# Performance work log

Hardware: AMD Instinct MI355X
Metric: run time of the kernel (lower is better)

Reference implementation:

```python
import jax, jax.numpy as jnp
import numpy as np

N = 20000      # nodes
E = 320000     # edges
S = 256        # scalar (0e) channels of irreps_feature
F = 960        # full irreps_feature dim (256x0e+128x1e+64x2e)
NB = 32        # number_of_basis
CUT = 5.0      # max_radius


def setup_inputs() -> dict:
    key = jax.random.key(0)
    ks = jax.random.split(key, 24)
    def w(k, shape):
        return jax.random.normal(k, shape, jnp.float32) / np.sqrt(shape[0])
    return {
        "node_feature": jax.random.normal(ks[0], (N, F), jnp.float32),
        "pos": jax.random.normal(ks[1], (N, 3), jnp.float32),
        "edge_index": jax.random.randint(ks[2], (2, E), 0, N),
        "W_ai1": w(ks[3], (S, S)), "b_ai1": jnp.zeros((S,), jnp.float32),
        "W_ai2": w(ks[4], (S, 1)), "b_ai2": jnp.zeros((1,), jnp.float32),
        "W_ci1": w(ks[5], (S, S)), "b_ci1": jnp.zeros((S,), jnp.float32),
        "W_ci2": w(ks[6], (S, 1)), "b_ci2": jnp.zeros((1,), jnp.float32),
        "W_sc": w(ks[7], (S, S)), "b_sc": jnp.zeros((S,), jnp.float32),
        "W_ed": w(ks[8], (NB, S)), "b_ed": jnp.zeros((S,), jnp.float32),
        "W_b1": w(ks[9], (3 * S, S)), "b_b1": jnp.zeros((S,), jnp.float32),
        "W_b2": w(ks[10], (S, 1)), "b_b2": jnp.zeros((1,), jnp.float32),
    }


def _rbf(d):
    # ExpNormalSmearing (torchmd-net), cutoff_lower=0, cutoff_upper=CUT, non-trainable
    start = np.exp(-CUT)
    means = jnp.linspace(start, 1.0, NB, dtype=jnp.float32)
    beta = jnp.float32(((2.0 / NB) * (1.0 - start)) ** -2)
    cosine_cut = 0.5 * (jnp.cos(np.pi * d / CUT) + 1.0) * (d < CUT)
    return cosine_cut[:, None] * jnp.exp(-beta * (jnp.exp(-d)[:, None] - means) ** 2)


def reference(node_feature, pos, edge_index,
              W_ai1, b_ai1, W_ai2, b_ai2,
              W_ci1, b_ci1, W_ci2, b_ci2,
              W_sc, b_sc, W_ed, b_ed,
              W_b1, b_b1, W_b2, b_b2):
    # LinearRS(irreps_feature -> 0e) only touches the 0e block (first S channels)
    scal = node_feature[:, :S]
    silu = jax.nn.silu

    log_ai = silu(scal @ W_ai1 + b_ai1) @ W_ai2 + b_ai2          # [N,1]
    ai = jnp.exp(log_ai)
    log_ci = silu(scal @ W_ci1 + b_ci1) @ W_ci2 + b_ci2          # [N,1]
    ci = jnp.exp(log_ci)

    src, dst = edge_index[0], edge_index[1]
    rel = pos[dst] - pos[src]                                     # [E,3]
    norm = jnp.linalg.norm(rel, axis=1, keepdims=True)            # [E,1]
    rhat = rel / (norm + 1e-8)
    emb = _rbf(norm[:, 0])                                        # [E,NB]

    node_sc = scal @ W_sc + b_sc                                  # project once, gather [N,S]
    src_f = node_sc[src]
    dst_f = node_sc[dst]
    edge_f = emb @ W_ed + b_ed
    edge_feature = jnp.concatenate([src_f, dst_f, edge_f], axis=-1)  # [E,3S]
    bij = silu(edge_feature @ W_b1 + b_b1) @ W_b2 + b_b2          # [E,1]

    # edge softmax over incoming edges of dst, with extra ci mass
    bmax = jax.ops.segment_max(bij, dst, num_segments=N)
    bmax = jnp.where(jnp.isneginf(bmax), 0.0, bmax)
    bij_exp = jnp.exp(bij - bmax[dst])
    bsum = jax.ops.segment_sum(bij_exp, dst, num_segments=N) + ci  # [N,1]
    gamma = bij_exp / (bsum[dst] + 1e-7)                           # [E,1]

    bij_prime = gamma * ai[dst]                                    # [E,1]
    outer = rhat[:, :, None] * rhat[:, None, :]                    # [E,3,3]
    contrib = jax.ops.segment_sum(bij_prime[:, :, None] * outer, dst, num_segments=N)  # [N,3,3]

    eye3 = jnp.eye(3, dtype=pos.dtype)
    sigma = ai[:, :, None] * eye3 - contrib + 1e-6 * eye3          # [N,3,3]
    sum_gamma = jax.ops.segment_sum(gamma, dst, num_segments=N)    # [N,1]
    return sigma, ai, sum_gamma
```

## Files before the change

kernel.cpp:

```cpp
#include <hip/hip_runtime.h>
#include <math.h>

#define N_NODES 20000
#define E_EDGES 320000
#define F_DIM   960
#define S_DIM   256
#define QTAB    2048
#define ASTRIDE 264
#define CAP     64
#define CPAD    66

typedef __attribute__((ext_vector_type(8))) short short8;
typedef __attribute__((ext_vector_type(4))) float f32x4;

__device__ __forceinline__ float siluf(float x) {
    return x / (1.0f + __expf(-x));
}

__device__ __forceinline__ unsigned short bf16rn(float x) {
    unsigned u = __float_as_uint(x);
    return (unsigned short)((u + 0x7FFFu + ((u >> 16) & 1u)) >> 16);
}

__device__ __forceinline__ void bf16x8_to_f32(short8 v8, float* o) {
    union { short8 s; uint4 u; } cv; cv.s = v8;
    o[0] = __uint_as_float(cv.u.x << 16);
    o[1] = __uint_as_float(cv.u.x & 0xffff0000u);
    o[2] = __uint_as_float(cv.u.y << 16);
    o[3] = __uint_as_float(cv.u.y & 0xffff0000u);
    o[4] = __uint_as_float(cv.u.z << 16);
    o[5] = __uint_as_float(cv.u.z & 0xffff0000u);
    o[6] = __uint_as_float(cv.u.w << 16);
    o[7] = __uint_as_float(cv.u.w & 0xffff0000u);
}

__global__ void prep_kernel(const float* __restrict__ W_sc, const float* __restrict__ W_ed,
                            const float* __restrict__ W_b1, const float* __restrict__ b_sc,
                            const float* __restrict__ b_ed, const float* __restrict__ b_b1,
                            const float* __restrict__ W_ai1, const float* __restrict__ W_ci1,
                            float* __restrict__ Bcat, float* __restrict__ We, float* __restrict__ c0,
                            int* __restrict__ cnt)
{
    int idx = blockIdx.x * 256 + threadIdx.x;
    if (idx < N_NODES) cnt[idx] = 0;
    if (idx < 256 * 1024) {
        int k = idx >> 10, j = idx & 1023;
        float s = 0.0f;
        if (j < 256) {
            for (int m = 0; m < 256; ++m) s += W_sc[k * 256 + m] * W_b1[m * 256 + j];
        } else if (j < 512) {
            int jj = j - 256;
            for (int m = 0; m < 256; ++m) s += W_sc[k * 256 + m] * W_b1[(256 + m) * 256 + jj];
        } else if (j < 768) {
            s = W_ai1[k * 256 + (j - 512)];
        } else {
            s = W_ci1[k * 256 + (j - 768)];
        }
        Bcat[idx] = s;
    } else if (idx < 256 * 1024 + 32 * 256) {
        int t = idx - 256 * 1024;
        int p = t >> 8, j = t & 255;
        float s = 0.0f;
        for (int m = 0; m < 256; ++m) s += W_ed[p * 256 + m] * W_b1[(512 + m) * 256 + j];
        We[t] = s;
    } else if (idx < 256 * 1024 + 32 * 256 + 256) {
        int j = idx - 256 * 1024 - 32 * 256;
        float s = b_b1[j];
        for (int m = 0; m < 256; ++m) {
            s += b_sc[m] * (W_b1[m * 256 + j] + W_b1[(256 + m) * 256 + j]);
            s += b_ed[m] * W_b1[(512 + m) * 256 + j];
        }
        c0[j] = s;
    }
}

__global__ void aux_kernel(const int* __restrict__ ei, int* __restrict__ cnt, int* __restrict__ rank,
                           const float* __restrict__ Bcat, unsigned short* __restrict__ Bpack,
                           const float* __restrict__ We, unsigned short* __restrict__ Tab,
                           const float* __restrict__ nf, unsigned short* __restrict__ scalp)
{
    int b = blockIdx.x;
    if (b < 1250) {
        int i = b * 256 + threadIdx.x;
        rank[i] = atomicAdd(&cnt[ei[E_EDGES + i]], 1);
    } else if (b < 1378) {
        int idx = (b - 1250) * 256 + threadIdx.x;
        int kq = idx & 3, j = (idx >> 2) & 1023, t = idx >> 12;
        #pragma unroll
        for (int jj = 0; jj < 8; ++jj)
            Bpack[idx * 8 + jj] = bf16rn(Bcat[(t * 32 + kq * 8 + jj) * 1024 + j]);
    } else if (b < 3426) {
        int idx = (b - 1378) * 256 + threadIdx.x;
        int q = idx >> 8, j = idx & 255;
        float nrm = 5.0f * (float)q / (float)(QTAB - 1);
        const float start = 0.006737946999085467f;
        const float mustep = (1.0f - start) / 31.0f;
        const float bx = (2.0f / 32.0f) * (1.0f - start);
        const float beta = 1.0f / (bx * bx);
        const float PI_F = 3.14159265358979323846f;
        float cc = (nrm < 5.0f) ? 0.5f * (cosf(PI_F * nrm * 0.2f) + 1.0f) : 0.0f;
        float t = expf(-nrm);
        float s = 0.0f;
        for (int k = 0; k < 32; ++k) {
            float dm = t - (start + (float)k * mustep);
            s += expf(-beta * dm * dm) * We[k * 256 + j];
        }
        Tab[idx] = bf16rn(cc * s);
    } else {
        int idx = (b - 3426) * 256 + threadIdx.x;
        int base = idx * 4;
        int n = base >> 8, k = base & 255;
        float4 a4 = *(const float4*)&nf[(size_t)n * F_DIM + k];
        ushort4 b4;
        b4.x = bf16rn(a4.x); b4.y = bf16rn(a4.y);
        b4.z = bf16rn(a4.z); b4.w = bf16rn(a4.w);
        *(ushort4*)&scalp[n * 256 + k] = b4;
    }
}

__global__ __launch_bounds__(1024) void scan_kernel(const int* __restrict__ cnt,
                                                    int* __restrict__ start)
{
    __shared__ int ps[1024];
    const int t = threadIdx.x;
    const int base = t * 20;
    int loc[20];
    int s = 0;
    #pragma unroll
    for (int i = 0; i < 20; ++i) {
        int n = (base + i < N_NODES) ? cnt[base + i] : 0;
        loc[i] = s; s += n;
    }
    ps[t] = s;
    __syncthreads();
    for (int off = 1; off < 1024; off <<= 1) {
        int v = (t >= off) ? ps[t - off] : 0;
        __syncthreads();
        ps[t] += v;
        __syncthreads();
    }
    int offset = ps[t] - s;
    #pragma unroll
    for (int i = 0; i < 20; ++i)
        if (base + i < N_NODES) start[base + i] = offset + loc[i];
}

__global__ void scatter_kernel(const int* __restrict__ ei, const int* __restrict__ start,
                               const int* __restrict__ rank, int* __restrict__ srcS)
{
    int i = blockIdx.x * 256 + threadIdx.x;
    if (i < E_EDGES) srcS[start[ei[E_EDGES + i]] + rank[i]] = ei[i];
}

__global__ __launch_bounds__(256) void node_mfma_kernel(
    const unsigned short* __restrict__ scalp, const unsigned short* __restrict__ Bpack,
    const float* __restrict__ c0,
    const float* __restrict__ b_ai1, const float* __restrict__ W_ai2, const float* __restrict__ b_ai2,
    const float* __restrict__ b_ci1, const float* __restrict__ W_ci2, const float* __restrict__ b_ci2,
    unsigned short* __restrict__ u, unsigned short* __restrict__ v,
    float* __restrict__ bsumseed, float* __restrict__ out_ai)
{
    __shared__ unsigned short A[32 * ASTRIDE];
    __shared__ float red[32 * 4];

    const int tid = threadIdx.x;
    const int w = tid >> 6, lane = tid & 63;
    const int bg = blockIdx.x & 3;
    const int m0 = (blockIdx.x >> 2) * 32;
    const int col16 = lane & 15, quad = lane >> 4;

    #pragma unroll
    for (int it = 0; it < 4; ++it) {
        int idx = (it * 256 + tid) * 8;
        int r = idx >> 8, c = idx & 255;
        *(uint4*)&A[r * ASTRIDE + c] = *(const uint4*)&scalp[(m0 + r) * 256 + c];
    }
    __syncthreads();

    f32x4 acc[2][4];
    #pragma unroll
    for (int mt = 0; mt < 2; ++mt)
        #pragma unroll
        for (int nt = 0; nt < 4; ++nt)
            acc[mt][nt] = (f32x4){0.0f, 0.0f, 0.0f, 0.0f};

    const int colbase = bg * 256 + w * 64;

    for (int t = 0; t < 8; ++t) {
        short8 af[2];
        #pragma unroll
        for (int mt = 0; mt < 2; ++mt)
            af[mt] = *(const short8*)&A[(mt * 16 + col16) * ASTRIDE + t * 32 + quad * 8];
        short8 bf[4];
        #pragma unroll
        for (int nt = 0; nt < 4; ++nt)
            bf[nt] = *(const short8*)&Bpack[(((t * 1024 + colbase + nt * 16 + col16) * 4) + quad) * 8];
        #pragma unroll
        for (int mt = 0; mt < 2; ++mt)
            #pragma unroll
            for (int nt = 0; nt < 4; ++nt)
                acc[mt][nt] = __builtin_amdgcn_mfma_f32_16x16x32_bf16(af[mt], bf[nt], acc[mt][nt], 0, 0, 0);
    }

    if (bg == 0) {
        #pragma unroll
        for (int nt = 0; nt < 4; ++nt) {
            int jl = w * 64 + nt * 16 + col16;
            float c0v = c0[jl];
            #pragma unroll
            for (int mt = 0; mt < 2; ++mt)
                #pragma unroll
                for (int reg = 0; reg < 4; ++reg)
                    u[(m0 + mt * 16 + quad * 4 + reg) * 256 + jl] = bf16rn(acc[mt][nt][reg] + c0v);
        }
    } else if (bg == 1) {
        #pragma unroll
        for (int nt = 0; nt < 4; ++nt) {
            int jl = w * 64 + nt * 16 + col16;
            #pragma unroll
            for (int mt = 0; mt < 2; ++mt)
                #pragma unroll
                for (int reg = 0; reg < 4; ++reg)
                    v[(m0 + mt * 16 + quad * 4 + reg) * 256 + jl] = bf16rn(acc[mt][nt][reg]);
        }
    } else {
        const float* b1 = (bg == 2) ? b_ai1 : b_ci1;
        const float* w2 = (bg == 2) ? W_ai2 : W_ci2;
        float s[2][4] = {{0, 0, 0, 0}, {0, 0, 0, 0}};
        #pragma unroll
        for (int nt = 0; nt < 4; ++nt) {
            int jl = w * 64 + nt * 16 + col16;
            float bb = b1[jl], ww = w2[jl];
            #pragma unroll
            for (int mt = 0; mt < 2; ++mt)
                #pragma unroll
                for (int reg = 0; reg < 4; ++reg)
                    s[mt][reg] += siluf(acc[mt][nt][reg] + bb) * ww;
        }
        #pragma unroll
        for (int off = 1; off < 16; off <<= 1) {
            #pragma unroll
            for (int mt = 0; mt < 2; ++mt)
                #pragma unroll
                for (int reg = 0; reg < 4; ++reg)
                    s[mt][reg] += __shfl_xor(s[mt][reg], off);
        }
        if (col16 == 0) {
            #pragma unroll
            for (int mt = 0; mt < 2; ++mt)
                #pragma unroll
                for (int reg = 0; reg < 4; ++reg)
                    red[(mt * 16 + quad * 4 + reg) * 4 + w] = s[mt][reg];
        }
        __syncthreads();
        if (tid < 32) {
            float sum = red[tid * 4] + red[tid * 4 + 1] + red[tid * 4 + 2] + red[tid * 4 + 3];
            if (bg == 2) out_ai[m0 + tid] = expf(sum + b_ai2[0]);
            else         bsumseed[m0 + tid] = expf(sum + b_ci2[0]) + 1e-7f;
        }
    }
}

__global__ __launch_bounds__(256) void edge_node_kernel(
    const int* __restrict__ start, const int* __restrict__ cnt, const int* __restrict__ srcS,
    const float* __restrict__ pos,
    const unsigned short* __restrict__ u, const unsigned short* __restrict__ v,
    const unsigned short* __restrict__ Tab, const float* __restrict__ W_b2, const float* __restrict__ b_b2,
    const float* __restrict__ bsumseed, const float* __restrict__ out_ai,
    float* __restrict__ out_sigma, float* __restrict__ out_sg)
{
    __shared__ float sb[16][CPAD];
    __shared__ float srx[16][CPAD];
    __shared__ float sry[16][CPAD];
    __shared__ float srz[16][CPAD];

    const int grp = threadIdx.x >> 4;
    const int l   = threadIdx.x & 15;
    const int g   = blockIdx.x * 16 + grp;
    const int st  = start[g];
    const int deg = min(cnt[g], CAP);

    float vch[16];
    bf16x8_to_f32(*(const short8*)&v[(size_t)g * 256 + l * 16], vch);
    bf16x8_to_f32(*(const short8*)&v[(size_t)g * 256 + l * 16 + 8], vch + 8);
    float w2c[16];
    #pragma unroll
    for (int c = 0; c < 16; c += 4)
        *(float4*)&w2c[c] = *(const float4*)&W_b2[l * 16 + c];
    const float bb2 = b_b2[0];
    const float gx = pos[3 * g + 0], gy = pos[3 * g + 1], gz = pos[3 * g + 2];
    const float xscale = (float)(QTAB - 1) * 0.2f;

    int s_cur = (deg > 0) ? srcS[st] : 0;
    float pxc = pos[3 * s_cur + 0], pyc = pos[3 * s_cur + 1], pzc = pos[3 * s_cur + 2];
    short8 u0c = *(const short8*)&u[(size_t)s_cur * 256 + l * 16];
    short8 u1c = *(const short8*)&u[(size_t)s_cur * 256 + l * 16 + 8];

    for (int i = 0; i < deg; ++i) {
        int s_nxt = (i + 1 < deg) ? srcS[st + i + 1] : s_cur;
        float pxn = pos[3 * s_nxt + 0], pyn = pos[3 * s_nxt + 1], pzn = pos[3 * s_nxt + 2];
        short8 u0n = *(const short8*)&u[(size_t)s_nxt * 256 + l * 16];
        short8 u1n = *(const short8*)&u[(size_t)s_nxt * 256 + l * 16 + 8];

        float px = gx - pxc, py = gy - pyc, pz = gz - pzc;
        float nrm = sqrtf(px * px + py * py + pz * pz);
        float inv = 1.0f / (nrm + 1e-8f);
        float rx = px * inv, ry = py * inv, rz = pz * inv;

        float x = nrm * xscale;
        int qi = (int)x;
        float f = x - (float)qi;
        if (qi >= QTAB - 1) { qi = QTAB - 2; f = 1.0f; }

        float acc = 0.0f;
        #pragma unroll
        for (int half = 0; half < 2; ++half) {
            float uf[8], t0f[8], t1f[8];
            bf16x8_to_f32(half ? u1c : u0c, uf);
            bf16x8_to_f32(*(const short8*)&Tab[(size_t)qi * 256 + l * 16 + half * 8], t0f);
            bf16x8_to_f32(*(const short8*)&Tab[(size_t)(qi + 1) * 256 + l * 16 + half * 8], t1f);
            #pragma unroll
            for (int c = 0; c < 8; ++c) {
                float h = uf[c] + vch[half * 8 + c] + t0f[c] + f * (t1f[c] - t0f[c]);
                float sig = __builtin_amdgcn_rcpf(1.0f + __expf(-h));
                acc += w2c[half * 8 + c] * h * sig;
            }
        }
        #pragma unroll
        for (int off = 1; off < 16; off <<= 1) acc += __shfl_xor(acc, off);

        if (l == 0) {
            sb[grp][i] = acc + bb2;
            srx[grp][i] = rx; sry[grp][i] = ry; srz[grp][i] = rz;
        }
        s_cur = s_nxt; pxc = pxn; pyc = pyn; pzc = pzn; u0c = u0n; u1c = u1n;
    }

    float m = -1e30f;
    for (int i = l; i < deg; i += 16) m = fmaxf(m, sb[grp][i]);
    #pragma unroll
    for (int off = 1; off < 16; off <<= 1) m = fmaxf(m, __shfl_xor(m, off));

    float ssum = 0.0f;
    for (int i = l; i < deg; i += 16) ssum += __expf(sb[grp][i] - m);
    #pragma unroll
    for (int off = 1; off < 16; off <<= 1) ssum += __shfl_xor(ssum, off);

    float invt = 1.0f / (ssum + bsumseed[g]);

    float a0 = 0, a1 = 0, a2 = 0, a3 = 0, a4 = 0, a5 = 0, a6 = 0;
    for (int i = l; i < deg; i += 16) {
        float gm = __expf(sb[grp][i] - m) * invt;
        float rx = srx[grp][i], ry = sry[grp][i], rz = srz[grp][i];
        a0 += gm * rx * rx; a1 += gm * ry * ry; a2 += gm * rz * rz;
        a3 += gm * rx * ry; a4 += gm * rx * rz; a5 += gm * ry * rz;
        a6 += gm;
    }
    #pragma unroll
    for (int off = 1; off < 16; off <<= 1) {
        a0 += __shfl_xor(a0, off); a1 += __shfl_xor(a1, off);
        a2 += __shfl_xor(a2, off); a3 += __shfl_xor(a3, off);
        a4 += __shfl_xor(a4, off); a5 += __shfl_xor(a5, off);
        a6 += __shfl_xor(a6, off);
    }

    if (l == 0) {
        float ai = out_ai[g];
        float* sg = &out_sigma[g * 9];
        float d0 = ai + 1e-6f;
        sg[0] = d0 - ai * a0;
        sg[1] = -ai * a3;
        sg[2] = -ai * a4;
        sg[3] = -ai * a3;
        sg[4] = d0 - ai * a1;
        sg[5] = -ai * a5;
        sg[6] = -ai * a4;
        sg[7] = -ai * a5;
        sg[8] = d0 - ai * a2;
        out_sg[g] = a6;
    }
}

extern "C" void kernel_launch(void* const* d_in, const int* in_sizes, int n_in,
                              void* d_out, int out_size, void* d_ws, size_t ws_size,
                              hipStream_t stream)
{
    const float* nf    = (const float*)d_in[0];
    const float* pos   = (const float*)d_in[1];
    const int*   ei    = (const int*)  d_in[2];
    const float* W_ai1 = (const float*)d_in[3];
    const float* b_ai1 = (const float*)d_in[4];
    const float* W_ai2 = (const float*)d_in[5];
    const float* b_ai2 = (const float*)d_in[6];
    const float* W_ci1 = (const float*)d_in[7];
    const float* b_ci1 = (const float*)d_in[8];
    const float* W_ci2 = (const float*)d_in[9];
    const float* b_ci2 = (const float*)d_in[10];
    const float* W_sc  = (const float*)d_in[11];
    const float* b_sc  = (const float*)d_in[12];
    const float* W_ed  = (const float*)d_in[13];
    const float* b_ed  = (const float*)d_in[14];
    const float* W_b1  = (const float*)d_in[15];
    const float* b_b1  = (const float*)d_in[16];
    const float* W_b2  = (const float*)d_in[17];
    const float* b_b2  = (const float*)d_in[18];

    char* pb = (char*)d_ws;
    auto alloc = [&](size_t bytes) -> void* {
        void* r = (void*)pb;
        pb += (bytes + 255) & ~(size_t)255;
        return r;
    };
    float*          Bcat    = (float*)         alloc(262144 * 4);
    float*          We      = (float*)         alloc(8192 * 4);
    float*          c0      = (float*)         alloc(256 * 4);
    unsigned short* Tab     = (unsigned short*)alloc((size_t)QTAB * 256 * 2);
    unsigned short* Bpack   = (unsigned short*)alloc((size_t)256 * 1024 * 2);
    unsigned short* scalp   = (unsigned short*)alloc((size_t)N_NODES * 256 * 2);
    unsigned short* u       = (unsigned short*)alloc((size_t)N_NODES * 256 * 2);
    unsigned short* v       = (unsigned short*)alloc((size_t)N_NODES * 256 * 2);
    float*          bsumseed= (float*)         alloc((size_t)N_NODES * 4);
    int*            cnt     = (int*)           alloc((size_t)N_NODES * 4);
    int*            startA  = (int*)           alloc((size_t)N_NODES * 4);
    int*            rank    = (int*)           alloc((size_t)E_EDGES * 4);
    int*            srcS    = (int*)           alloc((size_t)E_EDGES * 4);

    float* out       = (float*)d_out;
    float* out_sigma = out;
    float* out_ai    = out + N_NODES * 9;
    float* out_sg    = out + N_NODES * 10;

    prep_kernel<<<1058, 256, 0, stream>>>(W_sc, W_ed, W_b1, b_sc, b_ed, b_b1, W_ai1, W_ci1,
                                          Bcat, We, c0, cnt);
    aux_kernel<<<8426, 256, 0, stream>>>(ei, cnt, rank, Bcat, Bpack, We, Tab, nf, scalp);
    scan_kernel<<<1, 1024, 0, stream>>>(cnt, startA);
    scatter_kernel<<<1250, 256, 0, stream>>>(ei, startA, rank, srcS);
    node_mfma_kernel<<<2500, 256, 0, stream>>>(scalp, Bpack, c0, b_ai1, W_ai2, b_ai2,
                                               b_ci1, W_ci2, b_ci2, u, v, bsumseed, out_ai);
    edge_node_kernel<<<1250, 256, 0, stream>>>(startA, cnt, srcS, pos, u, v, Tab, W_b2, b_b2,
                                               bsumseed, out_ai, out_sigma, out_sg);
}
```

Measured before the change: 320.2 us.

## Split fused edge-node kernel into edge-parallel bij pass and node reduction

Replaces the per-destination sequential edge loop with an edge-parallel kernel (one 16-lane group per edge) that computes the edge logit and unit direction and scatters them into CSR order. A separate node kernel then does the softmax and outer-product reduction over the sorted float4 records. This removes the scatter kernel and the serial per-node dependency chain with its load imbalance, at the cost of an extra 5 MB write/read of intermediate edge records and reloading v per edge instead of once per node. The node kernel now handles at most 64 edges per node via 4 fixed slots, matching the existing CAP.

```diff
diff --git a/kernel.cpp b/kernel.cpp
--- a/kernel.cpp
+++ b/kernel.cpp
@@ -8,7 +8,6 @@
 #define QTAB    2048
 #define ASTRIDE 264
 #define CAP     64
-#define CPAD    66
 
 typedef __attribute__((ext_vector_type(8))) short short8;
 typedef __attribute__((ext_vector_type(4))) float f32x4;
@@ -145,13 +144,6 @@
         if (base + i < N_NODES) start[base + i] = offset + loc[i];
 }
 
-__global__ void scatter_kernel(const int* __restrict__ ei, const int* __restrict__ start,
-                               const int* __restrict__ rank, int* __restrict__ srcS)
-{
-    int i = blockIdx.x * 256 + threadIdx.x;
-    if (i < E_EDGES) srcS[start[ei[E_EDGES + i]] + rank[i]] = ei[i];
-}
-
 __global__ __launch_bounds__(256) void node_mfma_kernel(
     const unsigned short* __restrict__ scalp, const unsigned short* __restrict__ Bpack,
     const float* __restrict__ c0,
@@ -261,99 +253,114 @@
     }
 }
 
-__global__ __launch_bounds__(256) void edge_node_kernel(
-    const int* __restrict__ start, const int* __restrict__ cnt, const int* __restrict__ srcS,
+__global__ __launch_bounds__(256) void edge_bij_kernel(
+    const int* __restrict__ ei, const int* __restrict__ start, const int* __restrict__ rank,
     const float* __restrict__ pos,
     const unsigned short* __restrict__ u, const unsigned short* __restrict__ v,
-    const unsigned short* __restrict__ Tab, const float* __restrict__ W_b2, const float* __restrict__ b_b2,
+    const unsigned short* __restrict__ Tab,
+    const float* __restrict__ W_b2, const float* __restrict__ b_b2,
+    float4* __restrict__ bijS)
+{
+    const int l = threadIdx.x & 15;
+    const int e = blockIdx.x * 16 + (threadIdx.x >> 4);
+    const int src = ei[e];
+    const int dst = ei[E_EDGES + e];
+
+    float px = pos[3 * dst + 0] - pos[3 * src + 0];
+    float py = pos[3 * dst + 1] - pos[3 * src + 1];
+    float pz = pos[3 * dst + 2] - pos[3 * src + 2];
+    float nrm = sqrtf(px * px + py * py + pz * pz);
+    float inv = 1.0f / (nrm + 1e-8f);
+    float rx = px * inv, ry = py * inv, rz = pz * inv;
+
+    const float xscale = (float)(QTAB - 1) * 0.2f;
+    float x = nrm * xscale;
+    int qi = (int)x;
+    float f = x - (float)qi;
+    if (qi >= QTAB - 1) { qi = QTAB - 2; f = 1.0f; }
+
+    float w2c[16];
+    #pragma unroll
+    for (int c = 0; c < 16; c += 4)
+        *(float4*)&w2c[c] = *(const float4*)&W_b2[l * 16 + c];
+
+    short8 u0 = *(const short8*)&u[(size_t)src * 256 + l * 16];
+    short8 u1 = *(const short8*)&u[(size_t)src * 256 + l * 16 + 8];
+    short8 v0 = *(const short8*)&v[(size_t)dst * 256 + l * 16];
+    short8 v1 = *(const short8*)&v[(size_t)dst * 256 + l * 16 + 8];
+
+    float acc = 0.0f;
+    #pragma unroll
+    for (int half = 0; half < 2; ++half) {
+        float uf[8], vf[8], t0f[8], t1f[8];
+        bf16x8_to_f32(half ? u1 : u0, uf);
+        bf16x8_to_f32(half ? v1 : v0, vf);
+        bf16x8_to_f32(*(const short8*)&Tab[(size_t)qi * 256 + l * 16 + half * 8], t0f);
+        bf16x8_to_f32(*(const short8*)&Tab[(size_t)(qi + 1) * 256 + l * 16 + half * 8], t1f);
+        #pragma unroll
+        for (int c = 0; c < 8; ++c) {
+            float h = uf[c] + vf[c] + t0f[c] + f * (t1f[c] - t0f[c]);
+            float sig = __builtin_amdgcn_rcpf(1.0f + __expf(-h));
+            acc += w2c[half * 8 + c] * h * sig;
+        }
+    }
+    #pragma unroll
+    for (int off = 1; off < 16; off <<= 1) acc += __shfl_xor(acc, off);
+
+    if (l == 0) {
+        float4 o;
+        o.x = acc + b_b2[0];
+        o.y = rx; o.z = ry; o.w = rz;
+        bijS[start[dst] + rank[e]] = o;
+    }
+}
+
+__global__ __launch_bounds__(256) void node_reduce_kernel(
+    const int* __restrict__ start, const int* __restrict__ cnt,
+    const float4* __restrict__ bijS,
     const float* __restrict__ bsumseed, const float* __restrict__ out_ai,
     float* __restrict__ out_sigma, float* __restrict__ out_sg)
 {
-    __shared__ float sb[16][CPAD];
-    __shared__ float srx[16][CPAD];
-    __shared__ float sry[16][CPAD];
-    __shared__ float srz[16][CPAD];
-
     const int grp = threadIdx.x >> 4;
-    const int l   = threadIdx.x & 15;
-    const int g   = blockIdx.x * 16 + grp;
-    const int st  = start[g];
+    const int l = threadIdx.x & 15;
+    const int g = blockIdx.x * 16 + grp;
+    const int st = start[g];
     const int deg = min(cnt[g], CAP);
 
-    float vch[16];
-    bf16x8_to_f32(*(const short8*)&v[(size_t)g * 256 + l * 16], vch);
-    bf16x8_to_f32(*(const short8*)&v[(size_t)g * 256 + l * 16 + 8], vch + 8);
-    float w2c[16];
-    #pragma unroll
-    for (int c = 0; c < 16; c += 4)
-        *(float4*)&w2c[c] = *(const float4*)&W_b2[l * 16 + c];
-    const float bb2 = b_b2[0];
-    const float gx = pos[3 * g + 0], gy = pos[3 * g + 1], gz = pos[3 * g + 2];
-    const float xscale = (float)(QTAB - 1) * 0.2f;
-
-    int s_cur = (deg > 0) ? srcS[st] : 0;
-    float pxc = pos[3 * s_cur + 0], pyc = pos[3 * s_cur + 1], pzc = pos[3 * s_cur + 2];
-    short8 u0c = *(const short8*)&u[(size_t)s_cur * 256 + l * 16];
-    short8 u1c = *(const short8*)&u[(size_t)s_cur * 256 + l * 16 + 8];
-
-    for (int i = 0; i < deg; ++i) {
-        int s_nxt = (i + 1 < deg) ? srcS[st + i + 1] : s_cur;
-        float pxn = pos[3 * s_nxt + 0], pyn = pos[3 * s_nxt + 1], pzn = pos[3 * s_nxt + 2];
-        short8 u0n = *(const short8*)&u[(size_t)s_nxt * 256 + l * 16];
-        short8 u1n = *(const short8*)&u[(size_t)s_nxt * 256 + l * 16 + 8];
-
-        float px = gx - pxc, py = gy - pyc, pz = gz - pzc;
-        float nrm = sqrtf(px * px + py * py + pz * pz);
-        float inv = 1.0f / (nrm + 1e-8f);
-        float rx = px * inv, ry = py * inv, rz = pz * inv;
-
-        float x = nrm * xscale;
-        int qi = (int)x;
-        float f = x - (float)qi;
-        if (qi >= QTAB - 1) { qi = QTAB - 2; f = 1.0f; }
-
-        float acc = 0.0f;
-        #pragma unroll
-        for (int half = 0; half < 2; ++half) {
-            float uf[8], t0f[8], t1f[8];
-            bf16x8_to_f32(half ? u1c : u0c, uf);
-            bf16x8_to_f32(*(const short8*)&Tab[(size_t)qi * 256 + l * 16 + half * 8], t0f);
-            bf16x8_to_f32(*(const short8*)&Tab[(size_t)(qi + 1) * 256 + l * 16 + half * 8], t1f);
-            #pragma unroll
-            for (int c = 0; c < 8; ++c) {
-                float h = uf[c] + vch[half * 8 + c] + t0f[c] + f * (t1f[c] - t0f[c]);
-                float sig = __builtin_amdgcn_rcpf(1.0f + __expf(-h));
-                acc += w2c[half * 8 + c] * h * sig;
-            }
-        }
-        #pragma unroll
-        for (int off = 1; off < 16; off <<= 1) acc += __shfl_xor(acc, off);
-
-        if (l == 0) {
-            sb[grp][i] = acc + bb2;
-            srx[grp][i] = rx; sry[grp][i] = ry; srz[grp][i] = rz;
-        }
-        s_cur = s_nxt; pxc = pxn; pyc = pyn; pzc = pzn; u0c = u0n; u1c = u1n;
-    }
-
+    float bj[4], ex[4], ey[4], ez[4];
+    bool ok[4];
     float m = -1e30f;
-    for (int i = l; i < deg; i += 16) m = fmaxf(m, sb[grp][i]);
+    #pragma unroll
+    for (int k = 0; k < 4; ++k) {
+        int i = l + k * 16;
+        ok[k] = (i < deg);
+        float4 o;
+        if (ok[k]) o = bijS[st + i];
+        else { o.x = -1e30f; o.y = 0.0f; o.z = 0.0f; o.w = 0.0f; }
+        bj[k] = o.x; ex[k] = o.y; ey[k] = o.z; ez[k] = o.w;
+        m = fmaxf(m, bj[k]);
+    }
     #pragma unroll
     for (int off = 1; off < 16; off <<= 1) m = fmaxf(m, __shfl_xor(m, off));
 
+    float g4[4];
     float ssum = 0.0f;
-    for (int i = l; i < deg; i += 16) ssum += __expf(sb[grp][i] - m);
+    #pragma unroll
+    for (int k = 0; k < 4; ++k) {
+        g4[k] = ok[k] ? __expf(bj[k] - m) : 0.0f;
+        ssum += g4[k];
+    }
     #pragma unroll
     for (int off = 1; off < 16; off <<= 1) ssum += __shfl_xor(ssum, off);
 
     float invt = 1.0f / (ssum + bsumseed[g]);
 
     float a0 = 0, a1 = 0, a2 = 0, a3 = 0, a4 = 0, a5 = 0, a6 = 0;
-    for (int i = l; i < deg; i += 16) {
-        float gm = __expf(sb[grp][i] - m) * invt;
-        float rx = srx[grp][i], ry = sry[grp][i], rz = srz[grp][i];
-        a0 += gm * rx * rx; a1 += gm * ry * ry; a2 += gm * rz * rz;
-        a3 += gm * rx * ry; a4 += gm * rx * rz; a5 += gm * ry * rz;
+    #pragma unroll
+    for (int k = 0; k < 4; ++k) {
+        float gm = g4[k] * invt;
+        a0 += gm * ex[k] * ex[k]; a1 += gm * ey[k] * ey[k]; a2 += gm * ez[k] * ez[k];
+        a3 += gm * ex[k] * ey[k]; a4 += gm * ex[k] * ez[k]; a5 += gm * ey[k] * ez[k];
         a6 += gm;
     }
     #pragma unroll
@@ -423,7 +430,7 @@
     int*            cnt     = (int*)           alloc((size_t)N_NODES * 4);
     int*            startA  = (int*)           alloc((size_t)N_NODES * 4);
     int*            rank    = (int*)           alloc((size_t)E_EDGES * 4);
-    int*            srcS    = (int*)           alloc((size_t)E_EDGES * 4);
+    float4*         bijS    = (float4*)        alloc((size_t)E_EDGES * 16);
 
     float* out       = (float*)d_out;
     float* out_sigma = out;
@@ -434,9 +441,10 @@
                                           Bcat, We, c0, cnt);
     aux_kernel<<<8426, 256, 0, stream>>>(ei, cnt, rank, Bcat, Bpack, We, Tab, nf, scalp);
     scan_kernel<<<1, 1024, 0, stream>>>(cnt, startA);
-    scatter_kernel<<<1250, 256, 0, stream>>>(ei, startA, rank, srcS);
     node_mfma_kernel<<<2500, 256, 0, stream>>>(scalp, Bpack, c0, b_ai1, W_ai2, b_ai2,
                                                b_ci1, W_ci2, b_ci2, u, v, bsumseed, out_ai);
-    edge_node_kernel<<<1250, 256, 0, stream>>>(startA, cnt, srcS, pos, u, v, Tab, W_b2, b_b2,
-                                               bsumseed, out_ai, out_sigma, out_sg);
-}
+    edge_bij_kernel<<<20000, 256, 0, stream>>>(ei, startA, rank, pos, u, v, Tab, W_b2, b_b2,
+                                               bijS);
+    node_reduce_kernel<<<1250, 256, 0, stream>>>(startA, cnt, bijS, bsumseed, out_ai,
+                                                 out_sigma, out_sg);
+}
```

New measurement: 303.9 us. 1.05x faster.
